# Kernel optimization log

Measured on AMD Instinct MI355X. Metric: run time of the kernel, lower is better.

Reference implementation:

```python
import jax, jax.numpy as jnp
import numpy as np

B, LQ, LK, H = 4, 512, 512, 256


def setup_inputs() -> dict:
    key = jax.random.key(0)
    ks = jax.random.split(key, 8)
    s = 1.0 / np.sqrt(H)  # torch Linear init scale
    return {
        "query": jax.random.normal(ks[0], (B, LQ, H), dtype=jnp.float32),
        "values": jax.random.normal(ks[1], (B, LK, H), dtype=jnp.float32),
        "Wq": jax.random.uniform(ks[2], (H, H), jnp.float32, -s, s),
        "bq": jax.random.uniform(ks[3], (H,), jnp.float32, -s, s),
        "Wk": jax.random.uniform(ks[4], (H, H), jnp.float32, -s, s),
        "bk": jax.random.uniform(ks[5], (H,), jnp.float32, -s, s),
        "We": jax.random.uniform(ks[6], (H,), jnp.float32, -s, s),
        "be": jax.random.uniform(ks[7], (1,), jnp.float32, -s, s),
    }


def reference(query, values, Wq, bq, Wk, bk, We, be):
    # Linear projections (torch: x @ W.T + b)
    q = jnp.einsum("bqh,oh->bqo", query, Wq) + bq      # (B, Lq, H)
    k = jnp.einsum("bkh,oh->bko", values, Wk) + bk     # (B, Lk, H)
    # Additive attention energy: (B, Lq, Lk, H) broadcast add + tanh
    energy = jnp.tanh(q[:, :, None, :] + k[:, None, :, :])
    # energy_layer: Linear(H -> 1), squeeze -> scores (B, Lq, Lk)
    scores = jnp.einsum("bqkh,h->bqk", energy, We) + be[0]
    attention = jax.nn.softmax(scores, axis=-1)         # (B, Lq, Lk)
    context = jnp.einsum("bqk,bkh->bqh", attention, values)  # (B, Lq, H)
    return context, attention
```

## Files before the change

kernel.cpp:

```cpp
#include <hip/hip_runtime.h>


#define SCALE2 2.8853900817779268f

#if defined(__has_builtin)
#if __has_builtin(__builtin_amdgcn_exp2f)
#define FEXP2(x) __builtin_amdgcn_exp2f(x)
#endif
#if __has_builtin(__builtin_amdgcn_rcpf)
#define FRCP(x) __builtin_amdgcn_rcpf(x)
#endif
#endif
#ifndef FEXP2
#define FEXP2(x) exp2f(x)
#endif
#ifndef FRCP
#define FRCP(x) (1.0f/(x))
#endif

__global__ __launch_bounds__(512) void proj_kernel(
    const float* __restrict__ Q, const float* __restrict__ V,
    const float* __restrict__ Wq, const float* __restrict__ bq,
    const float* __restrict__ Wk, const float* __restrict__ bk,
    float* __restrict__ Eq, float* __restrict__ EkT)
{
  const int n0 = blockIdx.x * 64;
  const int o0 = blockIdx.y * 64;
  const bool isK = (blockIdx.z == 1);
  const float* X    = isK ? V  : Q;
  const float* W    = isK ? Wk : Wq;
  const float* bias = isK ? bk : bq;
  const int t  = threadIdx.x;
  const int tx = t & 15;
  const int ty = t >> 4;
  __shared__ float Xst[32][68];
  __shared__ float Wst[32][68];
  float acc[2][4] = {};
  const int sr = t >> 3, sc = (t & 7) << 2;
  float4 xv = *(const float4*)(X + (size_t)(n0 + sr) * 256 + sc);
  float4 wv = *(const float4*)(W + (size_t)(o0 + sr) * 256 + sc);
  for (int h0 = 0; h0 < 256; h0 += 32) {
    __syncthreads();
    Xst[sc  ][sr] = xv.x; Xst[sc+1][sr] = xv.y; Xst[sc+2][sr] = xv.z; Xst[sc+3][sr] = xv.w;
    Wst[sc  ][sr] = wv.x; Wst[sc+1][sr] = wv.y; Wst[sc+2][sr] = wv.z; Wst[sc+3][sr] = wv.w;
    __syncthreads();
    if (h0 < 224) {
      xv = *(const float4*)(X + (size_t)(n0 + sr) * 256 + h0 + 32 + sc);
      wv = *(const float4*)(W + (size_t)(o0 + sr) * 256 + h0 + 32 + sc);
    }
#pragma unroll 8
    for (int hh = 0; hh < 32; ++hh) {
      float2 a  = *(const float2*)&Xst[hh][ty*2];
      float4 bb = *(const float4*)&Wst[hh][tx*4];
      acc[0][0] = fmaf(a.x, bb.x, acc[0][0]); acc[0][1] = fmaf(a.x, bb.y, acc[0][1]);
      acc[0][2] = fmaf(a.x, bb.z, acc[0][2]); acc[0][3] = fmaf(a.x, bb.w, acc[0][3]);
      acc[1][0] = fmaf(a.y, bb.x, acc[1][0]); acc[1][1] = fmaf(a.y, bb.y, acc[1][1]);
      acc[1][2] = fmaf(a.y, bb.z, acc[1][2]); acc[1][3] = fmaf(a.y, bb.w, acc[1][3]);
    }
  }
  const float4 bv = *(const float4*)(bias + o0 + tx*4);
  float e[2][4];
#pragma unroll
  for (int i = 0; i < 2; ++i) {
    e[i][0] = FEXP2(SCALE2 * (acc[i][0] + bv.x));
    e[i][1] = FEXP2(SCALE2 * (acc[i][1] + bv.y));
    e[i][2] = FEXP2(SCALE2 * (acc[i][2] + bv.z));
    e[i][3] = FEXP2(SCALE2 * (acc[i][3] + bv.w));
  }
  if (!isK) {
#pragma unroll
    for (int i = 0; i < 2; ++i) {
      float4 st = {e[i][0], e[i][1], e[i][2], e[i][3]};
      *(float4*)(Eq + (size_t)(n0 + ty*2 + i) * 256 + o0 + tx*4) = st;
    }
  } else {
    const int b  = n0 >> 9;
    const int k0 = (n0 & 511) + ty*2;
#pragma unroll
    for (int j = 0; j < 4; ++j) {
      float2 st = {e[0][j], e[1][j]};
      *(float2*)(EkT + (size_t)b*131072 + (size_t)(o0 + tx*4 + j)*512 + k0) = st;
    }
  }
}

__global__ __launch_bounds__(256) void scores_kernel(
    const float* __restrict__ Eq, const float* __restrict__ EkT,
    const float* __restrict__ We, float* __restrict__ p0, float* __restrict__ p1)
{
  const int kt   = blockIdx.x & 7;
  const int half = blockIdx.x >> 3;
  const int qt = blockIdx.y;
  const int b  = blockIdx.z;
  const int t  = threadIdx.x;
  const int qi = t >> 4;
  const int k4 = (t & 15) << 2;

  __shared__ float ks[64][64];
  __shared__ float qs[16][68];

  const int hbase = half * 128;
  const float* eqbase = Eq  + (size_t)(b*512 + qt*16) * 256 + hbase;
  const float* ekbase = EkT + (size_t)b*131072 + (size_t)hbase*512 + (size_t)kt*64;
  const float* Weh    = We + hbase;
  float* sout = half ? p1 : p0;

  const int er = t >> 4, ec = (t & 15) << 2;
  float4 eqv, ekv[4];
  eqv = *(const float4*)(eqbase + (size_t)er*256 + ec);
#pragma unroll
  for (int rep = 0; rep < 4; ++rep) {
    int idx = rep*256 + t;
    int r = idx >> 4, c = (idx & 15) << 2;
    ekv[rep] = *(const float4*)(ekbase + (size_t)r*512 + c);
  }

  float a0 = 0.f, a1 = 0.f, a2 = 0.f, a3 = 0.f;

  for (int h0 = 0; h0 < 128; h0 += 64) {
    __syncthreads();
    *(float4*)&qs[er][ec] = eqv;
#pragma unroll
    for (int rep = 0; rep < 4; ++rep) {
      int idx = rep*256 + t;
      int r = idx >> 4, c = (idx & 15) << 2;
      *(float4*)&ks[r][c] = ekv[rep];
    }
    __syncthreads();
    if (h0 == 0) {
      eqv = *(const float4*)(eqbase + (size_t)er*256 + 64 + ec);
#pragma unroll
      for (int rep = 0; rep < 4; ++rep) {
        int idx = rep*256 + t;
        int r = idx >> 4, c = (idx & 15) << 2;
        ekv[rep] = *(const float4*)(ekbase + (size_t)(64 + r)*512 + c);
      }
    }
#pragma unroll 8
    for (int hh = 0; hh < 64; ++hh) {
      float w  = Weh[h0 + hh];
      float qv = qs[qi][hh];
      float4 kv = *(const float4*)&ks[hh][k4];
      float x0 = fmaf(qv, kv.x, 1.0f);
      float x1 = fmaf(qv, kv.y, 1.0f);
      float x2 = fmaf(qv, kv.z, 1.0f);
      float x3 = fmaf(qv, kv.w, 1.0f);
      float p01 = x0 * x1, p23 = x2 * x3;
      float r4  = FRCP(p01 * p23);
      float wr  = w * r4;
      float sw  = wr * p23, uw = wr * p01;
      a0 = fmaf(sw, x1, a0);
      a1 = fmaf(sw, x0, a1);
      a2 = fmaf(uw, x3, a2);
      a3 = fmaf(uw, x2, a3);
    }
  }
  float4 st = {a0, a1, a2, a3};
  *(float4*)(sout + (size_t)(b*512 + qt*16 + qi)*512 + kt*64 + k4) = st;
}

__global__ __launch_bounds__(512) void ctx_kernel(
    const float* __restrict__ values, const float* __restrict__ p0,
    const float* __restrict__ p1, float* __restrict__ attn,
    float* __restrict__ ctx)
{
  const int t    = threadIdx.x;
  const int row0 = blockIdx.x * 8;
  const int b    = row0 >> 9;
  __shared__ float ts[8][512];
  __shared__ float red[8][8][256];

#pragma unroll
  for (int rep = 0; rep < 2; ++rep) {
    int idx = rep*512 + t;
    int r = idx >> 7, c = (idx & 127) << 2;
    size_t off = (size_t)(row0 + r)*512 + c;
    float4 v0 = *(const float4*)(p0 + off);
    float4 v1 = *(const float4*)(p1 + off);
    float4 s = {v0.x+v1.x, v0.y+v1.y, v0.z+v1.z, v0.w+v1.w};
    *(float4*)&ts[r][c] = s;
  }
  __syncthreads();

  const int w = t >> 6, j = t & 63;
  {
    float v[8];
    float mn = 1e30f;
#pragma unroll
    for (int i = 0; i < 8; ++i) { v[i] = ts[w][j + 64*i]; mn = fminf(mn, v[i]); }
#pragma unroll
    for (int off = 32; off > 0; off >>= 1) mn = fminf(mn, __shfl_xor(mn, off, 64));
    float sum = 0.f;
#pragma unroll
    for (int i = 0; i < 8; ++i) { v[i] = FEXP2((mn - v[i]) * SCALE2); sum += v[i]; }
#pragma unroll
    for (int off = 32; off > 0; off >>= 1) sum += __shfl_xor(sum, off, 64);
    const float inv = 1.0f / sum;
    float* gp = attn + (size_t)(row0 + w) * 512 + j;
#pragma unroll
    for (int i = 0; i < 8; ++i) {
      float p = v[i] * inv;
      ts[w][j + 64*i] = p;
      gp[64*i] = p;
    }
  }
  __syncthreads();

  const int h4 = j << 2;
  const int wk0 = w * 64;
  const float* vwb = values + (size_t)b*131072 + (size_t)wk0*256 + h4;
  float4 acc[8];
#pragma unroll
  for (int r = 0; r < 8; ++r) acc[r] = (float4){0,0,0,0};

  float4 cv[4], nv[4];
#pragma unroll
  for (int jj = 0; jj < 4; ++jj) cv[jj] = *(const float4*)(vwb + (size_t)jj*256);

  for (int kq = 0; kq < 16; ++kq) {
    if (kq < 15) {
#pragma unroll
      for (int jj = 0; jj < 4; ++jj)
        nv[jj] = *(const float4*)(vwb + (size_t)((kq+1)*4 + jj)*256);
    }
    float4 a[8];
#pragma unroll
    for (int r = 0; r < 8; ++r) a[r] = *(const float4*)&ts[r][wk0 + kq*4];
#pragma unroll
    for (int jj = 0; jj < 4; ++jj) {
      float4 v4 = cv[jj];
#pragma unroll
      for (int r = 0; r < 8; ++r) {
        float ar = (jj == 0) ? a[r].x : (jj == 1) ? a[r].y : (jj == 2) ? a[r].z : a[r].w;
        acc[r].x = fmaf(ar, v4.x, acc[r].x);
        acc[r].y = fmaf(ar, v4.y, acc[r].y);
        acc[r].z = fmaf(ar, v4.z, acc[r].z);
        acc[r].w = fmaf(ar, v4.w, acc[r].w);
      }
    }
#pragma unroll
    for (int jj = 0; jj < 4; ++jj) cv[jj] = nv[jj];
  }

#pragma unroll
  for (int r = 0; r < 8; ++r) *(float4*)&red[w][r][h4] = acc[r];
  __syncthreads();
  {
    const int rr = t >> 6;
    const int hh4 = (t & 63) << 2;
    float4 s = *(const float4*)&red[0][rr][hh4];
#pragma unroll
    for (int ww = 1; ww < 8; ++ww) {
      float4 p = *(const float4*)&red[ww][rr][hh4];
      s.x += p.x; s.y += p.y; s.z += p.z; s.w += p.w;
    }
    *(float4*)(ctx + (size_t)(row0 + rr)*256 + hh4) = s;
  }
}

extern "C" void kernel_launch(void* const* d_in, const int* in_sizes, int n_in,
                              void* d_out, int out_size, void* d_ws, size_t ws_size,
                              hipStream_t stream)
{
  const float* query  = (const float*)d_in[0];
  const float* values = (const float*)d_in[1];
  const float* Wq     = (const float*)d_in[2];
  const float* bq     = (const float*)d_in[3];
  const float* Wk     = (const float*)d_in[4];
  const float* bk     = (const float*)d_in[5];
  const float* We     = (const float*)d_in[6];

  float* ctx  = (float*)d_out;
  float* attn = ctx + 4*512*256;
  float* Eq   = ctx;
  float* EkT  = (float*)d_ws;
  float* pt0  = EkT + 524288;
  float* pt1  = pt0 + 1048576;

  proj_kernel  <<<dim3(32, 4, 2), 512, 0, stream>>>(query, values, Wq, bq, Wk, bk, Eq, EkT);
  scores_kernel<<<dim3(16, 32, 4), 256, 0, stream>>>(Eq, EkT, We, pt0, pt1);
  ctx_kernel   <<<256, 512, 0, stream>>>(values, pt0, pt1, attn, ctx);
}
```

Baseline: 69.64 us.

## Register-tile scores kernel 4x4 with transposed Eq and four-way H split

The projection kernel now writes Eq transposed, like Ek, into workspace. The scores kernel computes a 4x4 q-by-k register tile per thread from 64x64 shared tiles, so each shared-memory load feeds more of the tanh-product math. H is split into four partial-sum buffers instead of two, and the launch uses a flat remapped grid of 1024 blocks. The context kernel then sums four partial buffers, which adds global read traffic and workspace in exchange for less LDS load pressure per FMA.

```diff
diff --git a/kernel.cpp b/kernel.cpp
--- a/kernel.cpp
+++ b/kernel.cpp
@@ -22,7 +22,7 @@
     const float* __restrict__ Q, const float* __restrict__ V,
     const float* __restrict__ Wq, const float* __restrict__ bq,
     const float* __restrict__ Wk, const float* __restrict__ bk,
-    float* __restrict__ Eq, float* __restrict__ EkT)
+    float* __restrict__ EqT, float* __restrict__ EkT)
 {
   const int n0 = blockIdx.x * 64;
   const int o0 = blockIdx.y * 64;
@@ -67,102 +67,87 @@
     e[i][2] = FEXP2(SCALE2 * (acc[i][2] + bv.z));
     e[i][3] = FEXP2(SCALE2 * (acc[i][3] + bv.w));
   }
-  if (!isK) {
-#pragma unroll
-    for (int i = 0; i < 2; ++i) {
-      float4 st = {e[i][0], e[i][1], e[i][2], e[i][3]};
-      *(float4*)(Eq + (size_t)(n0 + ty*2 + i) * 256 + o0 + tx*4) = st;
-    }
-  } else {
-    const int b  = n0 >> 9;
-    const int k0 = (n0 & 511) + ty*2;
-#pragma unroll
-    for (int j = 0; j < 4; ++j) {
-      float2 st = {e[0][j], e[1][j]};
-      *(float2*)(EkT + (size_t)b*131072 + (size_t)(o0 + tx*4 + j)*512 + k0) = st;
-    }
+  float* outT = isK ? EkT : EqT;
+  const int b  = n0 >> 9;
+  const int nl = (n0 & 511) + ty*2;
+#pragma unroll
+  for (int j = 0; j < 4; ++j) {
+    float2 st = {e[0][j], e[1][j]};
+    *(float2*)(outT + (size_t)b*131072 + (size_t)(o0 + tx*4 + j)*512 + nl) = st;
   }
 }
 
 __global__ __launch_bounds__(256) void scores_kernel(
-    const float* __restrict__ Eq, const float* __restrict__ EkT,
-    const float* __restrict__ We, float* __restrict__ p0, float* __restrict__ p1)
-{
-  const int kt   = blockIdx.x & 7;
-  const int half = blockIdx.x >> 3;
-  const int qt = blockIdx.y;
-  const int b  = blockIdx.z;
+    const float* __restrict__ EqT, const float* __restrict__ EkT,
+    const float* __restrict__ We, float* __restrict__ pt)
+{
+  const int flat = blockIdx.x;
+  const int u = flat & 7, v = flat >> 3;
+  const int z  = u*2 + (v >> 6);
+  const int qt = (v >> 3) & 7;
+  const int kt = v & 7;
+  const int b = z >> 2, half = z & 3;
+  const int h0 = half * 64;
   const int t  = threadIdx.x;
-  const int qi = t >> 4;
-  const int k4 = (t & 15) << 2;
-
-  __shared__ float ks[64][64];
-  __shared__ float qs[16][68];
-
-  const int hbase = half * 128;
-  const float* eqbase = Eq  + (size_t)(b*512 + qt*16) * 256 + hbase;
-  const float* ekbase = EkT + (size_t)b*131072 + (size_t)hbase*512 + (size_t)kt*64;
-  const float* Weh    = We + hbase;
-  float* sout = half ? p1 : p0;
-
-  const int er = t >> 4, ec = (t & 15) << 2;
-  float4 eqv, ekv[4];
-  eqv = *(const float4*)(eqbase + (size_t)er*256 + ec);
+  const int qr = t >> 4;
+  const int kr = t & 15;
+
+  __shared__ float qsT[64][64];
+  __shared__ float ks [64][64];
+
+  const float* eqb = EqT + (size_t)b*131072 + (size_t)h0*512 + qt*64;
+  const float* ekb = EkT + (size_t)b*131072 + (size_t)h0*512 + kt*64;
+
 #pragma unroll
   for (int rep = 0; rep < 4; ++rep) {
     int idx = rep*256 + t;
     int r = idx >> 4, c = (idx & 15) << 2;
-    ekv[rep] = *(const float4*)(ekbase + (size_t)r*512 + c);
-  }
-
-  float a0 = 0.f, a1 = 0.f, a2 = 0.f, a3 = 0.f;
-
-  for (int h0 = 0; h0 < 128; h0 += 64) {
-    __syncthreads();
-    *(float4*)&qs[er][ec] = eqv;
-#pragma unroll
-    for (int rep = 0; rep < 4; ++rep) {
-      int idx = rep*256 + t;
-      int r = idx >> 4, c = (idx & 15) << 2;
-      *(float4*)&ks[r][c] = ekv[rep];
-    }
-    __syncthreads();
-    if (h0 == 0) {
-      eqv = *(const float4*)(eqbase + (size_t)er*256 + 64 + ec);
-#pragma unroll
-      for (int rep = 0; rep < 4; ++rep) {
-        int idx = rep*256 + t;
-        int r = idx >> 4, c = (idx & 15) << 2;
-        ekv[rep] = *(const float4*)(ekbase + (size_t)(64 + r)*512 + c);
-      }
-    }
-#pragma unroll 8
-    for (int hh = 0; hh < 64; ++hh) {
-      float w  = Weh[h0 + hh];
-      float qv = qs[qi][hh];
-      float4 kv = *(const float4*)&ks[hh][k4];
-      float x0 = fmaf(qv, kv.x, 1.0f);
-      float x1 = fmaf(qv, kv.y, 1.0f);
-      float x2 = fmaf(qv, kv.z, 1.0f);
-      float x3 = fmaf(qv, kv.w, 1.0f);
+    *(float4*)&qsT[r][c] = *(const float4*)(eqb + (size_t)r*512 + c);
+    *(float4*)&ks [r][c] = *(const float4*)(ekb + (size_t)r*512 + c);
+  }
+  __syncthreads();
+
+  float a[4][4];
+#pragma unroll
+  for (int i = 0; i < 4; ++i)
+#pragma unroll
+    for (int j = 0; j < 4; ++j) a[i][j] = 0.f;
+
+#pragma unroll 4
+  for (int hh = 0; hh < 64; ++hh) {
+    const float w = We[h0 + hh];
+    const float4 qv = *(const float4*)&qsT[hh][qr*4];
+    const float4 kv = *(const float4*)&ks [hh][kr*4];
+    const float qa[4] = {qv.x, qv.y, qv.z, qv.w};
+#pragma unroll
+    for (int i = 0; i < 4; ++i) {
+      float x0 = fmaf(qa[i], kv.x, 1.0f);
+      float x1 = fmaf(qa[i], kv.y, 1.0f);
+      float x2 = fmaf(qa[i], kv.z, 1.0f);
+      float x3 = fmaf(qa[i], kv.w, 1.0f);
       float p01 = x0 * x1, p23 = x2 * x3;
       float r4  = FRCP(p01 * p23);
       float wr  = w * r4;
       float sw  = wr * p23, uw = wr * p01;
-      a0 = fmaf(sw, x1, a0);
-      a1 = fmaf(sw, x0, a1);
-      a2 = fmaf(uw, x3, a2);
-      a3 = fmaf(uw, x2, a3);
-    }
-  }
-  float4 st = {a0, a1, a2, a3};
-  *(float4*)(sout + (size_t)(b*512 + qt*16 + qi)*512 + kt*64 + k4) = st;
+      a[i][0] = fmaf(sw, x1, a[i][0]);
+      a[i][1] = fmaf(sw, x0, a[i][1]);
+      a[i][2] = fmaf(uw, x3, a[i][2]);
+      a[i][3] = fmaf(uw, x2, a[i][3]);
+    }
+  }
+
+  float* sout = pt + (size_t)half*1048576
+                   + (size_t)(b*512 + qt*64 + qr*4)*512 + kt*64 + kr*4;
+#pragma unroll
+  for (int i = 0; i < 4; ++i) {
+    float4 st = {a[i][0], a[i][1], a[i][2], a[i][3]};
+    *(float4*)(sout + (size_t)i*512) = st;
+  }
 }
 
 __global__ __launch_bounds__(512) void ctx_kernel(
-    const float* __restrict__ values, const float* __restrict__ p0,
-    const float* __restrict__ p1, float* __restrict__ attn,
-    float* __restrict__ ctx)
+    const float* __restrict__ values, const float* __restrict__ pt,
+    float* __restrict__ attn, float* __restrict__ ctx)
 {
   const int t    = threadIdx.x;
   const int row0 = blockIdx.x * 8;
@@ -175,9 +160,12 @@
     int idx = rep*512 + t;
     int r = idx >> 7, c = (idx & 127) << 2;
     size_t off = (size_t)(row0 + r)*512 + c;
-    float4 v0 = *(const float4*)(p0 + off);
-    float4 v1 = *(const float4*)(p1 + off);
-    float4 s = {v0.x+v1.x, v0.y+v1.y, v0.z+v1.z, v0.w+v1.w};
+    float4 v0 = *(const float4*)(pt + off);
+    float4 v1 = *(const float4*)(pt + 1048576 + off);
+    float4 v2 = *(const float4*)(pt + 2097152 + off);
+    float4 v3 = *(const float4*)(pt + 3145728 + off);
+    float4 s = {v0.x+v1.x+v2.x+v3.x, v0.y+v1.y+v2.y+v3.y,
+                v0.z+v1.z+v2.z+v3.z, v0.w+v1.w+v2.w+v3.w};
     *(float4*)&ts[r][c] = s;
   }
   __syncthreads();
@@ -272,12 +260,11 @@
 
   float* ctx  = (float*)d_out;
   float* attn = ctx + 4*512*256;
-  float* Eq   = ctx;
-  float* EkT  = (float*)d_ws;
-  float* pt0  = EkT + 524288;
-  float* pt1  = pt0 + 1048576;
-
-  proj_kernel  <<<dim3(32, 4, 2), 512, 0, stream>>>(query, values, Wq, bq, Wk, bk, Eq, EkT);
-  scores_kernel<<<dim3(16, 32, 4), 256, 0, stream>>>(Eq, EkT, We, pt0, pt1);
-  ctx_kernel   <<<256, 512, 0, stream>>>(values, pt0, pt1, attn, ctx);
-}
+  float* EqT  = (float*)d_ws;
+  float* EkT  = EqT + 524288;
+  float* pt   = EkT + 524288;
+
+  proj_kernel  <<<dim3(32, 4, 2), 512, 0, stream>>>(query, values, Wq, bq, Wk, bk, EqT, EkT);
+  scores_kernel<<<1024, 256, 0, stream>>>(EqT, EkT, We, pt);
+  ctx_kernel   <<<256, 512, 0, stream>>>(values, pt, attn, ctx);
+}
```

After: 65.00 us. 6.7% less time.
